# Kernel optimization log

Hardware: AMD Instinct MI355X
Metric: run time of the kernel (lower is better)

Reference implementation:

```python
import jax, jax.numpy as jnp
import numpy as np

NEG_INF = -1e9


def _rotate_half(x):
    h = x.shape[-1] // 2
    return jnp.concatenate([-x[..., h:], x[..., :h]], axis=-1)


def setup_inputs() -> dict:
    key = jax.random.key(0)
    ks = jax.random.split(key, 6)
    V, P, D, H = 4, 2048, 1280, 16
    hd = D // H
    return {
        "hidden_states": jax.random.normal(ks[0], (V, P, D), jnp.float32),
        "rope_cache": jax.random.normal(ks[1], (V, P, 1, 2 * hd), jnp.float32),
        "valid_lens": jax.random.randint(ks[2], (V,), 0, P, jnp.int32),
        "w_qkv": jax.random.normal(ks[3], (D, 3 * D), jnp.float32) * (D ** -0.5),
        "b_qkv": jnp.zeros((3 * D,), jnp.float32),
        "w_proj": jax.random.normal(ks[4], (D, D), jnp.float32) * (D ** -0.5),
        "b_proj": jnp.zeros((D,), jnp.float32),
        "n_heads": 16,
    }


def reference(hidden_states, rope_cache, valid_lens, w_qkv, b_qkv, w_proj, b_proj, n_heads):
    V, P, D = hidden_states.shape
    H = n_heads
    hd = D // H
    # fused QKV: (V, P, 3, H, hd)
    qkv = (hidden_states @ w_qkv + b_qkv).reshape(V, P, 3, H, hd)
    q, k, v = qkv[:, :, 0], qkv[:, :, 1], qkv[:, :, 2]  # each (V, P, H, hd)
    # 2D RoPE via precomputed cos/sin cache (V, P, 1, 2*hd)
    cos = rope_cache[..., :hd]
    sin = rope_cache[..., hd:]
    q = q * cos + _rotate_half(q) * sin
    k = k * cos + _rotate_half(k) * sin
    # attention with per-vision key padding mask (BlockMask equivalent)
    scale = hd ** -0.5
    scores = jnp.einsum("vqhd,vkhd->vhqk", q, k) * scale
    lens = jnp.maximum(valid_lens, 1)
    key_mask = jnp.arange(P)[None, :] < lens[:, None]  # (V, P)
    scores = jnp.where(key_mask[:, None, None, :], scores, NEG_INF)
    attn = jax.nn.softmax(scores, axis=-1)
    out = jnp.einsum("vhqk,vkhd->vqhd", attn, v).reshape(V, P, D)
    return out @ w_proj + b_proj
```

## Files before the change

### kernel.cpp

```cpp
#include <hip/hip_runtime.h>

typedef unsigned short u16;
typedef short bf16x8 __attribute__((ext_vector_type(8)));
typedef float f32x4 __attribute__((ext_vector_type(4)));

#define DEV __device__ __forceinline__

DEV float b2f(u16 u) { union { unsigned i; float f; } x; x.i = ((unsigned)u) << 16; return x.f; }
DEV u16 f2b(float f) {
  union { float f; unsigned i; } x; x.f = f;
  unsigned r = x.i + 0x7fffu + ((x.i >> 16) & 1u);
  return (u16)(r >> 16);
}

DEV float exp2g(float x) { return __builtin_amdgcn_exp2f(x); }

#define GLDS(gp, lp) __builtin_amdgcn_global_load_lds( \
    (const __attribute__((address_space(1))) void*)(gp), \
    (__attribute__((address_space(3))) void*)(lp), 16, 0, 0)

constexpr float QSCALE = 0.11180339887498949f * 1.4426950408889634f;

__global__ __launch_bounds__(256) void prep_k(const float* __restrict__ hidden,
    u16* __restrict__ Ah, const float* __restrict__ wq, u16* __restrict__ Btq)
{
  __shared__ u16 tile[64 * 40];
  int b = blockIdx.x, tid = threadIdx.x;
  if (b < 5120) {
    int i = (b * 256 + tid) * 8;
    f32x4 a = *(const f32x4*)(hidden + i);
    f32x4 c = *(const f32x4*)(hidden + i + 4);
    bf16x8 o;
#pragma unroll
    for (int j = 0; j < 4; ++j) { o[j] = (short)f2b(a[j]); o[4 + j] = (short)f2b(c[j]); }
    *(bf16x8*)(Ah + i) = o;
  } else {
    int tb = b - 5120;
    int bx = tb % 60, by = tb / 60;
    const int Kd = 1280, Nd = 3840;
    int k0 = by * 32, n0 = bx * 64;
#pragma unroll
    for (int t = 0; t < 2; ++t) {
      int c = t * 256 + tid;
      int k_l = c >> 4, n_l = (c & 15) << 2;
      f32x4 vv = *(const f32x4*)(wq + (size_t)(k0 + k_l) * Nd + n0 + n_l);
#pragma unroll
      for (int j = 0; j < 4; ++j) tile[(n_l + j) * 40 + k_l] = f2b(vv[j]);
    }
    __syncthreads();
    int n_l = tid >> 2, kc = (tid & 3) << 3;
    bf16x8 vv = *(const bf16x8*)(tile + n_l * 40 + kc);
    *(bf16x8*)(Btq + (size_t)(n0 + n_l) * Kd + k0 + kc) = vv;
  }
}

template<int MODE>
__global__ __launch_bounds__(256) void gemm_k(const u16* __restrict__ A,
    const u16* __restrict__ Bt, const float* __restrict__ bias,
    u16* __restrict__ Oq, u16* __restrict__ Ok, u16* __restrict__ Ov,
    float* __restrict__ Of, const int* __restrict__ lens, int M, int N, int K)
{
  __shared__ u16 Asm[128 * 64];
  __shared__ u16 Bsm[128 * 64];
  const int tid = threadIdx.x;
  const int w = tid >> 6, lane = tid & 63, quad = lane >> 4, l16 = lane & 15;
  const int wm = w >> 1, wn = w & 1;
  const int m0 = blockIdx.y * 128, n0 = blockIdx.x * 128;

  if (MODE == 0) {
    if (n0 >= 1280) {
      int vv = m0 >> 11, p0 = m0 & 2047;
      int len = lens[vv]; if (len < 1) len = 1;
      if (p0 >= len) return;
    }
  }

  const int srow = tid >> 3, spc = tid & 7;

  const f32x4 zero4 = {0.f, 0.f, 0.f, 0.f};
  f32x4 acc[4][4];
#pragma unroll
  for (int i = 0; i < 4; ++i)
#pragma unroll
    for (int j = 0; j < 4; ++j) acc[i][j] = zero4;

  for (int k0 = 0; k0 < K; k0 += 64) {
    __syncthreads();
#pragma unroll
    for (int g = 0; g < 4; ++g) {
      int r = g * 32 + srow;
      int q = spc ^ (r & 7);
      GLDS(A + (size_t)(m0 + r) * K + k0 + q * 8, Asm + r * 64 + spc * 8);
      GLDS(Bt + (size_t)(n0 + r) * K + k0 + q * 8, Bsm + r * 64 + spc * 8);
    }
    __syncthreads();
#pragma unroll
    for (int ks = 0; ks < 2; ++ks) {
      bf16x8 af[4], bfr[4];
#pragma unroll
      for (int mi = 0; mi < 4; ++mi) {
        int lr = wm * 64 + mi * 16 + l16;
        int ph = (ks * 4 + quad) ^ (lr & 7);
        af[mi] = *(const bf16x8*)(Asm + lr * 64 + ph * 8);
      }
#pragma unroll
      for (int ni = 0; ni < 4; ++ni) {
        int nr = wn * 64 + ni * 16 + l16;
        int ph = (ks * 4 + quad) ^ (nr & 7);
        bfr[ni] = *(const bf16x8*)(Bsm + nr * 64 + ph * 8);
      }
#pragma unroll
      for (int mi = 0; mi < 4; ++mi)
#pragma unroll
        for (int ni = 0; ni < 4; ++ni)
          acc[mi][ni] = __builtin_amdgcn_mfma_f32_16x16x32_bf16(af[mi], bfr[ni], acc[mi][ni], 0, 0, 0);
    }
  }

#pragma unroll
  for (int mi = 0; mi < 4; ++mi) {
#pragma unroll
    for (int ni = 0; ni < 4; ++ni) {
      int n = n0 + wn * 64 + ni * 16 + l16;
      float bb = bias[n];
#pragma unroll
      for (int r = 0; r < 4; ++r) {
        int m = m0 + wm * 64 + mi * 16 + quad * 4 + r;
        float val = acc[mi][ni][r] + bb;
        if (MODE == 0) {
          int t = n / 1280, rr = n - t * 1280;
          int hh = rr / 80, dd = rr - hh * 80;
          int vv = m >> 11, p = m & 2047;
          int vh = vv * 16 + hh;
          if (t == 0)      Oq[(size_t)(vh * 2048 + p) * 80 + dd] = f2b(val);
          else if (t == 1) Ok[(size_t)(vh * 2048 + p) * 80 + dd] = f2b(val);
          else             Ov[((size_t)vh * 80 + dd) * 2048 + p] = f2b(val);
        } else {
          Of[(size_t)m * N + n] = val;
        }
      }
    }
  }
}

__global__ __launch_bounds__(256) void rope_proj_k(u16* __restrict__ Q, u16* __restrict__ K,
    const float* __restrict__ rope, const float* __restrict__ wp, u16* __restrict__ Btp)
{
  __shared__ u16 tile[64 * 40];
  int b = blockIdx.x, tid = threadIdx.x;
  if (b < 40960) {
    constexpr int TOT = 4 * 16 * 2048 * 40;
    int idx = b * 256 + tid;
    int which = idx >= TOT ? 1 : 0;
    int r = which ? idx - TOT : idx;
    int d = r % 40;
    int t1 = r / 40;
    int p = t1 & 2047;
    int vv = t1 >> 15;
    u16* buf = which ? K : Q;
    size_t base = (size_t)t1 * 80;
    int rc = (vv * 2048 + p) * 160;
    float x0 = b2f(buf[base + d]), x1 = b2f(buf[base + d + 40]);
    float c0 = rope[rc + d], c1 = rope[rc + d + 40];
    float s0 = rope[rc + 80 + d], s1 = rope[rc + 80 + d + 40];
    float y0 = x0 * c0 - x1 * s0;
    float y1 = x1 * c1 + x0 * s1;
    if (!which) { y0 *= QSCALE; y1 *= QSCALE; }
    buf[base + d] = f2b(y0);
    buf[base + d + 40] = f2b(y1);
  } else {
    int tb = b - 40960;
    int bx = tb % 20, by = tb / 20;
    const int Kd = 1280, Nd = 1280;
    int k0 = by * 32, n0 = bx * 64;
#pragma unroll
    for (int t = 0; t < 2; ++t) {
      int c = t * 256 + tid;
      int k_l = c >> 4, n_l = (c & 15) << 2;
      f32x4 vv = *(const f32x4*)(wp + (size_t)(k0 + k_l) * Nd + n0 + n_l);
#pragma unroll
      for (int j = 0; j < 4; ++j) tile[(n_l + j) * 40 + k_l] = f2b(vv[j]);
    }
    __syncthreads();
    int n_l = tid >> 2, kc = (tid & 3) << 3;
    bf16x8 vv = *(const bf16x8*)(tile + n_l * 40 + kc);
    *(bf16x8*)(Btp + (size_t)(n0 + n_l) * Kd + k0 + kc) = vv;
  }
}

__global__ __launch_bounds__(256) void attn_k(const u16* __restrict__ Q,
    const u16* __restrict__ K, const u16* __restrict__ V,
    const int* __restrict__ lens, u16* __restrict__ O, const u16* __restrict__ zbuf)
{
  __shared__ u16 Ksm[64 * 96];
  __shared__ u16 Vt[96 * 64];
  __shared__ u16 Psm[4][16 * 72];
  const int v = blockIdx.z, h = blockIdx.y, q0 = blockIdx.x * 64;
  const int tid = threadIdx.x, w = tid >> 6, lane = tid & 63;
  const int quad = lane >> 4, l16 = lane & 15;
  int len = lens[v]; if (len < 1) len = 1;
  const int vh = v * 16 + h;

  if (tid < 128) {
    int row = 80 + (tid >> 3), pc = tid & 7;
    short val = (row == 80) ? (short)0x3F80 : (short)0;
    bf16x8 v8 = {val, val, val, val, val, val, val, val};
    *(bf16x8*)(Vt + row * 64 + pc * 8) = v8;
  }

  const bf16x8 zero8 = {0, 0, 0, 0, 0, 0, 0, 0};
  bf16x8 qf[3];
  {
    const u16* qp = Q + (size_t)(vh * 2048 + q0 + w * 16 + l16) * 80 + quad * 8;
    qf[0] = *(const bf16x8*)(qp);
    qf[1] = *(const bf16x8*)(qp + 32);
    qf[2] = (quad < 2) ? *(const bf16x8*)(qp + 64) : zero8;
  }

  const u16* kp[3]; int kstr[3];
#pragma unroll
  for (int t = 0; t < 3; ++t) {
    int L = w * 192 + t * 64 + lane;
    int key = L / 12, pc = L - key * 12;
    int q = (pc < 8) ? (pc ^ (key & 7)) : (8 + ((pc - 8) ^ (key & 3)));
    bool valid = q < 10;
    kp[t] = valid ? (K + (size_t)(vh * 2048 + key) * 80 + q * 8) : zbuf;
    kstr[t] = valid ? 5120 : 0;
  }
  const u16* vp[3];
#pragma unroll
  for (int t = 0; t < 3; ++t) {
    int seg = w + t * 4;
    int d = seg * 8 + (lane >> 3), pc = lane & 7;
    int q = pc ^ (d & 7);
    vp[t] = V + ((size_t)vh * 80 + d) * 2048 + q * 8;
  }

  const f32x4 zero4 = {0.f, 0.f, 0.f, 0.f};
  f32x4 o[6];
#pragma unroll
  for (int i = 0; i < 6; ++i) o[i] = zero4;
  float m_run[4] = {-3e38f, -3e38f, -3e38f, -3e38f};

  for (int key0 = 0; key0 < len; key0 += 64) {
    __syncthreads();
#pragma unroll
    for (int t = 0; t < 3; ++t) {
      GLDS(kp[t], Ksm + (w * 192 + t * 64) * 8);
      kp[t] += kstr[t];
    }
#pragma unroll
    for (int t = 0; t < 3; ++t) {
      int seg = w + t * 4;
      if (seg < 10) { GLDS(vp[t], Vt + seg * 512); vp[t] += 64; }
    }
    __syncthreads();

    f32x4 s[4];
#pragma unroll
    for (int i = 0; i < 4; ++i) s[i] = zero4;
    __builtin_amdgcn_s_setprio(1);
#pragma unroll
    for (int ks = 0; ks < 3; ++ks) {
      int ph = (ks < 2) ? ((ks * 4 + quad) ^ (l16 & 7)) : (8 + (quad ^ (l16 & 3)));
#pragma unroll
      for (int ni = 0; ni < 4; ++ni) {
        bf16x8 kb = *(const bf16x8*)(Ksm + (ni * 16 + l16) * 96 + ph * 8);
        s[ni] = __builtin_amdgcn_mfma_f32_16x16x32_bf16(qf[ks], kb, s[ni], 0, 0, 0);
      }
    }
    __builtin_amdgcn_s_setprio(0);

    if (key0 + 64 > len) {
#pragma unroll
      for (int ni = 0; ni < 4; ++ni) {
        int key = key0 + ni * 16 + l16;
        if (key >= len) {
#pragma unroll
          for (int r = 0; r < 4; ++r) s[ni][r] = -1e9f;
        }
      }
    }
    float mx[4];
#pragma unroll
    for (int r = 0; r < 4; ++r) mx[r] = fmaxf(fmaxf(s[0][r], s[1][r]), fmaxf(s[2][r], s[3][r]));
#pragma unroll
    for (int off = 1; off < 16; off <<= 1)
#pragma unroll
      for (int r = 0; r < 4; ++r) mx[r] = fmaxf(mx[r], __shfl_xor(mx[r], off, 64));

    int grow = (mx[0] > m_run[0] + 8.f) | (mx[1] > m_run[1] + 8.f) |
               (mx[2] > m_run[2] + 8.f) | (mx[3] > m_run[3] + 8.f);
    if (__any(grow)) {
      float alpha[4];
#pragma unroll
      for (int r = 0; r < 4; ++r) {
        float mn = fmaxf(m_run[r], mx[r]);
        alpha[r] = exp2g(m_run[r] - mn);
        m_run[r] = mn;
      }
#pragma unroll
      for (int ni = 0; ni < 6; ++ni)
#pragma unroll
        for (int r = 0; r < 4; ++r) o[ni][r] *= alpha[r];
    }

#pragma unroll
    for (int ni = 0; ni < 4; ++ni)
#pragma unroll
      for (int r = 0; r < 4; ++r) s[ni][r] = exp2g(s[ni][r] - m_run[r]);

#pragma unroll
    for (int ni = 0; ni < 4; ++ni) {
      unsigned w0, w1;
      asm("v_cvt_pk_bf16_f32 %0, %1, %2" : "=v"(w0) : "v"(s[ni][0]), "v"(s[ni][1]));
      asm("v_cvt_pk_bf16_f32 %0, %1, %2" : "=v"(w1) : "v"(s[ni][2]), "v"(s[ni][3]));
      u16* pp = &Psm[w][ni * 16 + l16];
      pp[(quad * 4 + 0) * 72] = (u16)w0;
      pp[(quad * 4 + 1) * 72] = (u16)(w0 >> 16);
      pp[(quad * 4 + 2) * 72] = (u16)w1;
      pp[(quad * 4 + 3) * 72] = (u16)(w1 >> 16);
    }

    __builtin_amdgcn_s_setprio(1);
#pragma unroll
    for (int ks = 0; ks < 2; ++ks) {
      bf16x8 pa = *(const bf16x8*)(&Psm[w][l16 * 72 + ks * 32 + quad * 8]);
      int ph = (ks * 4 + quad) ^ (l16 & 7);
#pragma unroll
      for (int ni = 0; ni < 6; ++ni) {
        bf16x8 vb = *(const bf16x8*)(Vt + (ni * 16 + l16) * 64 + ph * 8);
        o[ni] = __builtin_amdgcn_mfma_f32_16x16x32_bf16(pa, vb, o[ni], 0, 0, 0);
      }
    }
    __builtin_amdgcn_s_setprio(0);
  }
  float inv[4];
#pragma unroll
  for (int r = 0; r < 4; ++r) {
    float l = __shfl(o[5][r], (lane & 48), 64);
    inv[r] = 1.0f / l;
  }
#pragma unroll
  for (int ni = 0; ni < 5; ++ni)
#pragma unroll
    for (int r = 0; r < 4; ++r) {
      int qq = q0 + w * 16 + quad * 4 + r;
      O[((size_t)(v * 2048 + qq) * 16 + h) * 80 + ni * 16 + l16] = f2b(o[ni][r] * inv[r]);
    }
}

extern "C" void kernel_launch(void* const* d_in, const int* in_sizes, int n_in,
                              void* d_out, int out_size, void* d_ws, size_t ws_size,
                              hipStream_t stream) {
  const float* hidden = (const float*)d_in[0];
  const float* rope   = (const float*)d_in[1];
  const int*   lens   = (const int*)d_in[2];
  const float* w_qkv  = (const float*)d_in[3];
  const float* b_qkv  = (const float*)d_in[4];
  const float* w_proj = (const float*)d_in[5];
  const float* b_proj = (const float*)d_in[6];
  float* out = (float*)d_out;
  char* ws = (char*)d_ws;
  u16* Ah = (u16*)(ws);
  u16* Bt = (u16*)(ws + 20971520);
  u16* Qb = (u16*)(ws + 30801920);
  u16* Kb = (u16*)(ws + 51773440);
  u16* Vb = (u16*)(ws + 72744960);
  u16* At = Ah;
  u16* Bp = Bt;

  prep_k<<<7520, 256, 0, stream>>>(hidden, Ah, w_qkv, Bt);
  gemm_k<0><<<dim3(30, 64), 256, 0, stream>>>(Ah, Bt, b_qkv, Qb, Kb, Vb, nullptr, lens, 8192, 3840, 1280);
  rope_proj_k<<<41760, 256, 0, stream>>>(Qb, Kb, rope, w_proj, Bp);
  attn_k<<<dim3(32, 16, 4), 256, 0, stream>>>(Qb, Kb, Vb, lens, At, (const u16*)b_qkv);
  gemm_k<1><<<dim3(10, 64), 256, 0, stream>>>(At, Bp, b_proj, nullptr, nullptr, nullptr, out, lens, 8192, 1280, 1280);
}
```

Measured before the change: 381.8 us.

## Vectorize RoPE, register-prefetch K/V tiles, use DPP row-max reduction

Three changes land together. The RoPE pass now has each thread handle 8 elements with 16-byte loads and stores, which cuts the launch from 41760 blocks to 5920. In attention, K/V tiles are loaded into registers one iteration ahead and then written to LDS, replacing the direct global-to-LDS loads, so the global latency overlaps the MFMA and softmax work. The 16-lane row max now uses DPP instructions instead of shuffles. The costs are higher register pressure in attention and an extra register-to-LDS write step.

```diff
diff --git a/kernel.cpp b/kernel.cpp
--- a/kernel.cpp
+++ b/kernel.cpp
@@ -14,6 +14,13 @@
 }
 
 DEV float exp2g(float x) { return __builtin_amdgcn_exp2f(x); }
+
+template<int CTRL>
+DEV float dppmax(float x) {
+  int t = __builtin_amdgcn_update_dpp(__builtin_bit_cast(int, x),
+                                      __builtin_bit_cast(int, x), CTRL, 0xf, 0xf, false);
+  return fmaxf(x, __builtin_bit_cast(float, t));
+}
 
 #define GLDS(gp, lp) __builtin_amdgcn_global_load_lds( \
     (const __attribute__((address_space(1))) void*)(gp), \
@@ -148,28 +155,42 @@
 {
   __shared__ u16 tile[64 * 40];
   int b = blockIdx.x, tid = threadIdx.x;
-  if (b < 40960) {
-    constexpr int TOT = 4 * 16 * 2048 * 40;
+  if (b < 5120) {
     int idx = b * 256 + tid;
-    int which = idx >= TOT ? 1 : 0;
-    int r = which ? idx - TOT : idx;
-    int d = r % 40;
-    int t1 = r / 40;
-    int p = t1 & 2047;
-    int vv = t1 >> 15;
+    int which = idx >= 655360 ? 1 : 0;
+    int r = which ? idx - 655360 : idx;
+    int row = r / 5, c = r - row * 5;
+    int d0 = c * 8;
+    int p = row & 2047, vv = row >> 15;
     u16* buf = which ? K : Q;
-    size_t base = (size_t)t1 * 80;
+    size_t base = (size_t)row * 80;
     int rc = (vv * 2048 + p) * 160;
-    float x0 = b2f(buf[base + d]), x1 = b2f(buf[base + d + 40]);
-    float c0 = rope[rc + d], c1 = rope[rc + d + 40];
-    float s0 = rope[rc + 80 + d], s1 = rope[rc + 80 + d + 40];
-    float y0 = x0 * c0 - x1 * s0;
-    float y1 = x1 * c1 + x0 * s1;
-    if (!which) { y0 *= QSCALE; y1 *= QSCALE; }
-    buf[base + d] = f2b(y0);
-    buf[base + d + 40] = f2b(y1);
+    bf16x8 x0 = *(const bf16x8*)(buf + base + d0);
+    bf16x8 x1 = *(const bf16x8*)(buf + base + 40 + d0);
+    f32x4 c0a = *(const f32x4*)(rope + rc + d0);
+    f32x4 c0b = *(const f32x4*)(rope + rc + d0 + 4);
+    f32x4 c1a = *(const f32x4*)(rope + rc + 40 + d0);
+    f32x4 c1b = *(const f32x4*)(rope + rc + 44 + d0);
+    f32x4 s0a = *(const f32x4*)(rope + rc + 80 + d0);
+    f32x4 s0b = *(const f32x4*)(rope + rc + 84 + d0);
+    f32x4 s1a = *(const f32x4*)(rope + rc + 120 + d0);
+    f32x4 s1b = *(const f32x4*)(rope + rc + 124 + d0);
+    float sc = which ? 1.0f : QSCALE;
+    bf16x8 y0, y1;
+#pragma unroll
+    for (int j = 0; j < 8; ++j) {
+      float xa = b2f((u16)x0[j]), xb = b2f((u16)x1[j]);
+      float cc0 = j < 4 ? c0a[j & 3] : c0b[j & 3];
+      float cc1 = j < 4 ? c1a[j & 3] : c1b[j & 3];
+      float ss0 = j < 4 ? s0a[j & 3] : s0b[j & 3];
+      float ss1 = j < 4 ? s1a[j & 3] : s1b[j & 3];
+      y0[j] = (short)f2b((xa * cc0 - xb * ss0) * sc);
+      y1[j] = (short)f2b((xb * cc1 + xa * ss1) * sc);
+    }
+    *(bf16x8*)(buf + base + d0) = y0;
+    *(bf16x8*)(buf + base + 40 + d0) = y1;
   } else {
-    int tb = b - 40960;
+    int tb = b - 5120;
     int bx = tb % 20, by = tb / 20;
     const int Kd = 1280, Nd = 1280;
     int k0 = by * 32, n0 = bx * 64;
@@ -228,13 +249,29 @@
     kstr[t] = valid ? 5120 : 0;
   }
   const u16* vp[3];
+  bool vok[3];
 #pragma unroll
   for (int t = 0; t < 3; ++t) {
     int seg = w + t * 4;
     int d = seg * 8 + (lane >> 3), pc = lane & 7;
     int q = pc ^ (d & 7);
     vp[t] = V + ((size_t)vh * 80 + d) * 2048 + q * 8;
-  }
+    vok[t] = seg < 10;
+  }
+
+  f32x4 kreg[3], vreg[3];
+#define ISSUE_KV() do { \
+  _Pragma("unroll") \
+  for (int t = 0; t < 3; ++t) { kreg[t] = *(const f32x4*)(kp[t]); kp[t] += kstr[t]; } \
+  _Pragma("unroll") \
+  for (int t = 0; t < 3; ++t) { if (vok[t]) { vreg[t] = *(const f32x4*)(vp[t]); vp[t] += 64; } } \
+} while (0)
+#define WRITE_KV() do { \
+  _Pragma("unroll") \
+  for (int t = 0; t < 3; ++t) *(f32x4*)(Ksm + (w * 192 + t * 64 + lane) * 8) = kreg[t]; \
+  _Pragma("unroll") \
+  for (int t = 0; t < 3; ++t) { if (vok[t]) *(f32x4*)(Vt + (w + t * 4) * 512 + lane * 8) = vreg[t]; } \
+} while (0)
 
   const f32x4 zero4 = {0.f, 0.f, 0.f, 0.f};
   f32x4 o[6];
@@ -242,19 +279,12 @@
   for (int i = 0; i < 6; ++i) o[i] = zero4;
   float m_run[4] = {-3e38f, -3e38f, -3e38f, -3e38f};
 
+  ISSUE_KV();
   for (int key0 = 0; key0 < len; key0 += 64) {
     __syncthreads();
-#pragma unroll
-    for (int t = 0; t < 3; ++t) {
-      GLDS(kp[t], Ksm + (w * 192 + t * 64) * 8);
-      kp[t] += kstr[t];
-    }
-#pragma unroll
-    for (int t = 0; t < 3; ++t) {
-      int seg = w + t * 4;
-      if (seg < 10) { GLDS(vp[t], Vt + seg * 512); vp[t] += 64; }
-    }
-    __syncthreads();
+    WRITE_KV();
+    __syncthreads();
+    if (key0 + 64 < len) ISSUE_KV();
 
     f32x4 s[4];
 #pragma unroll
@@ -283,11 +313,13 @@
     }
     float mx[4];
 #pragma unroll
-    for (int r = 0; r < 4; ++r) mx[r] = fmaxf(fmaxf(s[0][r], s[1][r]), fmaxf(s[2][r], s[3][r]));
-#pragma unroll
-    for (int off = 1; off < 16; off <<= 1)
-#pragma unroll
-      for (int r = 0; r < 4; ++r) mx[r] = fmaxf(mx[r], __shfl_xor(mx[r], off, 64));
+    for (int r = 0; r < 4; ++r) {
+      mx[r] = fmaxf(fmaxf(s[0][r], s[1][r]), fmaxf(s[2][r], s[3][r]));
+      mx[r] = dppmax<0xB1>(mx[r]);
+      mx[r] = dppmax<0x4E>(mx[r]);
+      mx[r] = dppmax<0x124>(mx[r]);
+      mx[r] = dppmax<0x128>(mx[r]);
+    }
 
     int grow = (mx[0] > m_run[0] + 8.f) | (mx[1] > m_run[1] + 8.f) |
                (mx[2] > m_run[2] + 8.f) | (mx[3] > m_run[3] + 8.f);
@@ -348,6 +380,8 @@
       int qq = q0 + w * 16 + quad * 4 + r;
       O[((size_t)(v * 2048 + qq) * 16 + h) * 80 + ni * 16 + l16] = f2b(o[ni][r] * inv[r]);
     }
+#undef ISSUE_KV
+#undef WRITE_KV
 }
 
 extern "C" void kernel_launch(void* const* d_in, const int* in_sizes, int n_in,
@@ -372,7 +406,7 @@
 
   prep_k<<<7520, 256, 0, stream>>>(hidden, Ah, w_qkv, Bt);
   gemm_k<0><<<dim3(30, 64), 256, 0, stream>>>(Ah, Bt, b_qkv, Qb, Kb, Vb, nullptr, lens, 8192, 3840, 1280);
-  rope_proj_k<<<41760, 256, 0, stream>>>(Qb, Kb, rope, w_proj, Bp);
+  rope_proj_k<<<5920, 256, 0, stream>>>(Qb, Kb, rope, w_proj, Bp);
   attn_k<<<dim3(32, 16, 4), 256, 0, stream>>>(Qb, Kb, Vb, lens, At, (const u16*)b_qkv);
   gemm_k<1><<<dim3(10, 64), 256, 0, stream>>>(At, Bp, b_proj, nullptr, nullptr, nullptr, out, lens, 8192, 1280, 1280);
 }
```

Result: faster. 371.7 us (-2.6%).
